# Kernel tuning notes

Measured on AMD Instinct MI355X. Metric: run time of the kernel, lower is better.

The kernel has to match this reference:

```python
import jax, jax.numpy as jnp
import numpy as np

IN_FEATURES = 1024
OUT_FEATURES = 1024
BATCH = 32
SEQ = 1024
EPS = 1e-8


def setup_inputs() -> dict:
    key = jax.random.key(0)
    k1, k2, k3 = jax.random.split(key, 3)
    Efou = jax.random.normal(k1, (BATCH, SEQ, IN_FEATURES), dtype=jnp.float32)
    y = jax.random.normal(k2, (BATCH, IN_FEATURES), dtype=jnp.float32)
    weight = jax.random.normal(k3, (IN_FEATURES, OUT_FEATURES), dtype=jnp.float32)
    return {"Efou": Efou, "y": y, "weight": weight}


def reference(Efou, y, weight):
    # scale = 1/sqrt(in_features)
    scale = 1.0 / np.sqrt(np.float32(weight.shape[0]))
    ys = y * scale  # (b, i) == per-sample column scaling of weight
    # Demodulation norm: sum_i (scale*W[i,o]*y[b,i])^2 = (ys^2) @ (W^2)
    d = jax.lax.rsqrt(jnp.einsum('bi,io->bo', ys * ys, weight * weight) + EPS)  # (b, o)
    # Efou @ (scale*W*y*d) == ((Efou*ys) @ W) * d  -- same math, avoids (b,i,o) weight
    out = jnp.einsum('bsi,io->bso', Efou * ys[:, None, :], weight) * d[:, None, :]
    return out
```

## Files before the change

### kernel.cpp

```cpp
#include <hip/hip_runtime.h>

#define AS1 __attribute__((address_space(1)))
#define AS3 __attribute__((address_space(3)))

typedef __bf16 bf16x8 __attribute__((ext_vector_type(8)));
typedef float f32x4 __attribute__((ext_vector_type(4)));

__device__ __forceinline__ unsigned short f2bf(float f) {
  union { float f; unsigned u; } v; v.f = f;
  unsigned u = v.u;
  unsigned r = (u + 0x7fffu + ((u >> 16) & 1u)) >> 16;
  return (unsigned short)r;
}

__global__ __launch_bounds__(256) void dcalc_a_kernel(const float* __restrict__ y,
                                                      const float* __restrict__ W,
                                                      float* __restrict__ partial) {
  __shared__ float ysq[32][32];
  const int o = blockIdx.x * 256 + threadIdx.x;
  const int i0 = blockIdx.y * 32;
  for (int e = threadIdx.x; e < 1024; e += 256) {
    int il = e >> 5, b = e & 31;
    float t = y[b * 1024 + i0 + il] * 0.03125f;
    ysq[il][b] = t * t;
  }
  __syncthreads();

  f32x4 acc[8] = {};
#pragma unroll
  for (int il = 0; il < 32; ++il) {
    float w = W[(size_t)(i0 + il) * 1024 + o];
    float w2 = w * w;
#pragma unroll
    for (int b4 = 0; b4 < 8; ++b4) {
      f32x4 q = *(const f32x4*)&ysq[il][b4 * 4];
#pragma unroll
      for (int k = 0; k < 4; ++k) acc[b4][k] = fmaf(q[k], w2, acc[b4][k]);
    }
  }
  float* p = partial + (size_t)blockIdx.y * 32768 + o;
#pragma unroll
  for (int b4 = 0; b4 < 8; ++b4)
#pragma unroll
    for (int k = 0; k < 4; ++k) p[(b4 * 4 + k) * 1024] = acc[b4][k];
}

__global__ __launch_bounds__(256) void dcalc_b_kernel(const float* __restrict__ partial,
                                                      float* __restrict__ dmod) {
  const int bo = blockIdx.x * 256 + threadIdx.x;
  float acc = 0.f;
#pragma unroll 8
  for (int is = 0; is < 32; ++is) acc += partial[(size_t)is * 32768 + bo];
  dmod[bo] = rsqrtf(acc + 1e-8f);
}

__global__ void wconv_kernel(const float* __restrict__ W,
                             unsigned short* __restrict__ WT) {
  __shared__ float t[32][33];
  const int tx = threadIdx.x;
  const int ty = threadIdx.y;
  const int i0 = blockIdx.y * 32;
  const int o0 = blockIdx.x * 32;
#pragma unroll
  for (int k = 0; k < 4; ++k)
    t[ty + k * 8][tx] = W[(size_t)(i0 + ty + k * 8) * 1024 + o0 + tx];
  __syncthreads();
#pragma unroll
  for (int k = 0; k < 4; ++k)
    WT[(size_t)(o0 + ty + k * 8) * 1024 + i0 + tx] = f2bf(t[tx][ty + k * 8]);
}

__global__ __launch_bounds__(256) void xconv_kernel(const float4* __restrict__ E4,
                                                    const float* __restrict__ y,
                                                    unsigned short* __restrict__ X) {
  const size_t total = (size_t)8388608;
  for (size_t g = (size_t)blockIdx.x * blockDim.x + threadIdx.x; g < total;
       g += (size_t)gridDim.x * blockDim.x) {
    float4 v = E4[g];
    size_t e = g * 4;
    int i = (int)(e & 1023);
    int b = (int)(e >> 20);
    float4 yv = *(const float4*)(y + b * 1024 + i);
    ushort4 o;
    o.x = f2bf(v.x * yv.x * 0.03125f);
    o.y = f2bf(v.y * yv.y * 0.03125f);
    o.z = f2bf(v.z * yv.z * 0.03125f);
    o.w = f2bf(v.w * yv.w * 0.03125f);
    *(ushort4*)(X + e) = o;
  }
}

#define NT 16
#define LDS_TILE 65536

#define BAR __builtin_amdgcn_s_barrier()
#define LGKM0 asm volatile("s_waitcnt lgkmcnt(0)" ::: "memory")
#define VM(n) asm volatile("s_waitcnt vmcnt(" #n ")" ::: "memory")
#define SCHB __builtin_amdgcn_sched_barrier(0)
#define PRIO(x) __builtin_amdgcn_s_setprio(x)

#define STG_A(r, t, dst)                                                     \
  __builtin_amdgcn_global_load_lds(                                          \
      (const AS1 void*)(Xs + (size_t)(r) * 64 * 2048 + (t) * 128),           \
      (AS3 void*)((dst) + (r) * 8192 + sldso), 16, 0, 0)
#define STG_B(r, t, dst)                                                     \
  __builtin_amdgcn_global_load_lds(                                          \
      (const AS1 void*)(Ws + (size_t)(r) * 64 * 2048 + (t) * 128),           \
      (AS3 void*)((dst) + 32768 + (r) * 8192 + sldso), 16, 0, 0)

#define RD_A(mh, mi, kk)                                                     \
  (*(const bf16x8*)(Ab + (wr * 128 + ((mh) * 4 + (mi)) * 16 + l15) * 128 +   \
                    ((((kk) * 64 + lhi * 16)) ^ swz_rd)))
#define RD_B(nh, ni, kk)                                                     \
  (*(const bf16x8*)(Bb + (wc * 64 + ((nh) * 2 + (ni)) * 16 + l15) * 128 +    \
                    ((((kk) * 64 + lhi * 16)) ^ swz_rd)))

#define LD_A(mh)                                                             \
  { _Pragma("unroll") for (int mi = 0; mi < 4; ++mi)                         \
      _Pragma("unroll") for (int kk = 0; kk < 2; ++kk)                       \
        a[mi][kk] = RD_A(mh, mi, kk); }
#define LD_B(nh)                                                             \
  { _Pragma("unroll") for (int ni = 0; ni < 2; ++ni)                         \
      _Pragma("unroll") for (int kk = 0; kk < 2; ++kk)                       \
        bfr[ni][kk] = RD_B(nh, ni, kk); }

#define MM(mh, nh)                                                           \
  do {                                                                       \
    _Pragma("unroll") for (int mi = 0; mi < 4; ++mi)                         \
      _Pragma("unroll") for (int ni = 0; ni < 2; ++ni)                       \
        _Pragma("unroll") for (int kk = 0; kk < 2; ++kk)                     \
          acc[(mh) * 4 + mi][(nh) * 2 + ni] =                                \
              __builtin_amdgcn_mfma_f32_16x16x32_bf16(                       \
                  a[mi][kk], bfr[ni][kk], acc[(mh) * 4 + mi][(nh) * 2 + ni], \
                  0, 0, 0);                                                  \
  } while (0)

__global__ __launch_bounds__(512, 2) void gemm8_kernel(
    const unsigned short* __restrict__ X, const unsigned short* __restrict__ WT,
    const float* __restrict__ dmod, float* __restrict__ out) {
  extern __shared__ char lds[];
  const int tid = threadIdx.x;
  const int bid = blockIdx.x;
  const int wg = (bid & 7) * 64 + (bid >> 3);
  const int bm = wg >> 2, bn = wg & 3;
  const int m0 = bm * 256, n0 = bn * 256;

  const int w = tid >> 6, l = tid & 63;
  const int wr = w >> 2, wc = w & 3;
  const int l15 = l & 15, lhi = l >> 4;
  const int swz_rd = (l15 & 7) << 4;

  const int srow = tid >> 3;
  const int scb = ((tid & 7) << 4) ^ ((srow & 7) << 4);
  const char* Xs = (const char*)X + (size_t)(m0 + srow) * 2048 + scb;
  const char* Ws = (const char*)WT + (size_t)(n0 + srow) * 2048 + scb;
  const int sldso = tid * 16;

  f32x4 acc[8][4] = {};
  bf16x8 a[4][2], bfr[2][2];

  {
    char* d0 = lds;
    STG_A(0, 0, d0); STG_A(2, 0, d0); STG_B(0, 0, d0); STG_B(1, 0, d0);
    STG_B(2, 0, d0); STG_B(3, 0, d0); STG_A(1, 0, d0); STG_A(3, 0, d0);
  }
  VM(2);
  BAR;

  for (int t = 0; t < NT - 1; ++t) {
    const char* Ab = lds + (t & 1) * LDS_TILE;
    const char* Bb = Ab + 32768;
    char* dN = lds + ((t & 1) ^ 1) * LDS_TILE;
    const int t1 = t + 1;
    LD_A(0); LD_B(0);
    STG_A(0, t1, dN); STG_A(2, t1, dN);
    BAR; LGKM0; SCHB; PRIO(1); MM(0, 0); PRIO(0); SCHB; BAR;
    LD_B(1);
    STG_B(0, t1, dN); STG_B(1, t1, dN);
    BAR; LGKM0; SCHB; PRIO(1); MM(0, 1); PRIO(0); SCHB;
    VM(4);
    BAR;
    LD_A(1); LD_B(0);
    STG_B(2, t1, dN); STG_B(3, t1, dN);
    BAR; LGKM0; SCHB; PRIO(1); MM(1, 0); PRIO(0); SCHB; BAR;
    LD_B(1);
    STG_A(1, t1, dN); STG_A(3, t1, dN);
    BAR; LGKM0; SCHB; PRIO(1); MM(1, 1); PRIO(0); SCHB;
    VM(2);
    BAR;
  }

  {
    const char* Ab = lds + ((NT - 1) & 1) * LDS_TILE;
    const char* Bb = Ab + 32768;
    LD_A(0); LD_B(0);
    BAR; LGKM0; SCHB; PRIO(1); MM(0, 0); PRIO(0); SCHB; BAR;
    LD_B(1);
    BAR; LGKM0; SCHB; PRIO(1); MM(0, 1); PRIO(0); SCHB;
    VM(0);
    BAR;
    LD_A(1); LD_B(0);
    BAR; LGKM0; SCHB; PRIO(1); MM(1, 0); PRIO(0); SCHB; BAR;
    LD_B(1);
    BAR; LGKM0; SCHB; PRIO(1); MM(1, 1); PRIO(0); SCHB;
  }

  const int b = m0 >> 10;
  const int col0 = n0 + wc * 64 + l15;
  float dv[4];
#pragma unroll
  for (int nf = 0; nf < 4; ++nf) dv[nf] = dmod[b * 1024 + col0 + nf * 16];
#pragma unroll
  for (int mf = 0; mf < 8; ++mf) {
#pragma unroll
    for (int j = 0; j < 4; ++j) {
      const int row = m0 + wr * 128 + mf * 16 + lhi * 4 + j;
      float* orow = out + (size_t)row * 1024 + col0;
#pragma unroll
      for (int nf = 0; nf < 4; ++nf) orow[nf * 16] = acc[mf][nf][j] * dv[nf];
    }
  }
}

extern "C" void kernel_launch(void* const* d_in, const int* in_sizes, int n_in,
                              void* d_out, int out_size, void* d_ws, size_t ws_size,
                              hipStream_t stream) {
  const float* Efou = (const float*)d_in[0];
  const float* y    = (const float*)d_in[1];
  const float* W    = (const float*)d_in[2];
  float* out = (float*)d_out;

  unsigned short* X  = (unsigned short*)d_ws;
  unsigned short* WT = X + (size_t)32768 * 1024;
  float* dmod        = (float*)(WT + (size_t)1024 * 1024);
  float* dpart       = dmod + 32768;

  hipFuncSetAttribute((const void*)gemm8_kernel,
                      hipFuncAttributeMaxDynamicSharedMemorySize, 131072);

  dcalc_a_kernel<<<dim3(4, 32), 256, 0, stream>>>(y, W, dpart);
  dcalc_b_kernel<<<128, 256, 0, stream>>>(dpart, dmod);
  wconv_kernel<<<dim3(32, 32), dim3(32, 8), 0, stream>>>(W, WT);
  xconv_kernel<<<2048, 256, 0, stream>>>((const float4*)Efou, y, X);
  gemm8_kernel<<<512, 512, 131072, stream>>>(X, WT, dmod, out);
}
```

Before: 138.9 us.

## Fuse Efou scaling and bf16 conversion into the GEMM A-tile load path

Removes the separate xconv kernel that materialized a scaled bf16 copy of Efou in workspace. The GEMM now loads fp32 Efou rows into registers, multiplies them by the per-batch y scale kept in LDS, converts to bf16 and writes the swizzled A tile to LDS itself. Only the weight tiles still use direct global-to-LDS loads. This drops the write and re-read of the 64 MB intermediate, at the cost of heavier fp32 A traffic per tile (each tile is reread by several column blocks), extra registers, and a full vmcnt(0) wait every iteration that weakens prefetch overlap.

Measured after the change: 129.6 us. -6.7%, faster.

```diff
diff --git a/kernel.cpp b/kernel.cpp
--- a/kernel.cpp
+++ b/kernel.cpp
@@ -5,6 +5,7 @@
 
 typedef __bf16 bf16x8 __attribute__((ext_vector_type(8)));
 typedef float f32x4 __attribute__((ext_vector_type(4)));
+typedef unsigned short ushort8 __attribute__((ext_vector_type(8)));
 
 __device__ __forceinline__ unsigned short f2bf(float f) {
   union { float f; unsigned u; } v; v.f = f;
@@ -70,26 +71,6 @@
     WT[(size_t)(o0 + ty + k * 8) * 1024 + i0 + tx] = f2bf(t[tx][ty + k * 8]);
 }
 
-__global__ __launch_bounds__(256) void xconv_kernel(const float4* __restrict__ E4,
-                                                    const float* __restrict__ y,
-                                                    unsigned short* __restrict__ X) {
-  const size_t total = (size_t)8388608;
-  for (size_t g = (size_t)blockIdx.x * blockDim.x + threadIdx.x; g < total;
-       g += (size_t)gridDim.x * blockDim.x) {
-    float4 v = E4[g];
-    size_t e = g * 4;
-    int i = (int)(e & 1023);
-    int b = (int)(e >> 20);
-    float4 yv = *(const float4*)(y + b * 1024 + i);
-    ushort4 o;
-    o.x = f2bf(v.x * yv.x * 0.03125f);
-    o.y = f2bf(v.y * yv.y * 0.03125f);
-    o.z = f2bf(v.z * yv.z * 0.03125f);
-    o.w = f2bf(v.w * yv.w * 0.03125f);
-    *(ushort4*)(X + e) = o;
-  }
-}
-
 #define NT 16
 #define LDS_TILE 65536
 
@@ -99,14 +80,34 @@
 #define SCHB __builtin_amdgcn_sched_barrier(0)
 #define PRIO(x) __builtin_amdgcn_s_setprio(x)
 
-#define STG_A(r, t, dst)                                                     \
-  __builtin_amdgcn_global_load_lds(                                          \
-      (const AS1 void*)(Xs + (size_t)(r) * 64 * 2048 + (t) * 128),           \
-      (AS3 void*)((dst) + (r) * 8192 + sldso), 16, 0, 0)
 #define STG_B(r, t, dst)                                                     \
   __builtin_amdgcn_global_load_lds(                                          \
       (const AS1 void*)(Ws + (size_t)(r) * 64 * 2048 + (t) * 128),           \
       (AS3 void*)((dst) + 32768 + (r) * 8192 + sldso), 16, 0, 0)
+
+#define A_ISSUE(t)                                                           \
+  {                                                                          \
+    const float* asrc = Efou + (size_t)(m0 + argp * 4) * 1024 + (t) * 64 + k8; \
+    _Pragma("unroll") for (int rr = 0; rr < 4; ++rr) {                       \
+      pa[rr][0] = *(const f32x4*)(asrc + rr * 1024);                         \
+      pa[rr][1] = *(const f32x4*)(asrc + rr * 1024 + 4);                     \
+    }                                                                        \
+    yv[0] = *(const f32x4*)(ysS + (t) * 64 + k8);                            \
+    yv[1] = *(const f32x4*)(ysS + (t) * 64 + k8 + 4);                        \
+  }
+
+#define A_WRITE(dst)                                                         \
+  {                                                                          \
+    _Pragma("unroll") for (int rr = 0; rr < 4; ++rr) {                       \
+      const int row = argp * 4 + rr;                                         \
+      ushort8 ov;                                                            \
+      _Pragma("unroll") for (int q = 0; q < 4; ++q) {                        \
+        ov[q] = f2bf(pa[rr][0][q] * yv[0][q]);                               \
+        ov[q + 4] = f2bf(pa[rr][1][q] * yv[1][q]);                           \
+      }                                                                      \
+      *(ushort8*)((dst) + row * 128 + ((kslot * 16) ^ ((row & 7) << 4))) = ov; \
+    }                                                                        \
+  }
 
 #define RD_A(mh, mi, kk)                                                     \
   (*(const bf16x8*)(Ab + (wr * 128 + ((mh) * 4 + (mi)) * 16 + l15) * 128 +   \
@@ -135,37 +136,51 @@
                   0, 0, 0);                                                  \
   } while (0)
 
-__global__ __launch_bounds__(512, 2) void gemm8_kernel(
-    const unsigned short* __restrict__ X, const unsigned short* __restrict__ WT,
-    const float* __restrict__ dmod, float* __restrict__ out) {
+__global__ __launch_bounds__(512, 2) void gemmf_kernel(
+    const float* __restrict__ Efou, const float* __restrict__ y,
+    const unsigned short* __restrict__ WT, const float* __restrict__ dmod,
+    float* __restrict__ out) {
   extern __shared__ char lds[];
+  float* ysS = (float*)(lds + 2 * LDS_TILE);
+
   const int tid = threadIdx.x;
   const int bid = blockIdx.x;
   const int wg = (bid & 7) * 64 + (bid >> 3);
   const int bm = wg >> 2, bn = wg & 3;
   const int m0 = bm * 256, n0 = bn * 256;
+  const int b = m0 >> 10;
 
   const int w = tid >> 6, l = tid & 63;
   const int wr = w >> 2, wc = w & 3;
   const int l15 = l & 15, lhi = l >> 4;
   const int swz_rd = (l15 & 7) << 4;
 
+  const int kslot = tid & 7;
+  const int k8 = kslot * 8;
+  const int argp = tid >> 3;
+
   const int srow = tid >> 3;
   const int scb = ((tid & 7) << 4) ^ ((srow & 7) << 4);
-  const char* Xs = (const char*)X + (size_t)(m0 + srow) * 2048 + scb;
   const char* Ws = (const char*)WT + (size_t)(n0 + srow) * 2048 + scb;
   const int sldso = tid * 16;
 
   f32x4 acc[8][4] = {};
   bf16x8 a[4][2], bfr[2][2];
-
+  f32x4 pa[4][2], yv[2];
+
+  {
+    float2 yy = *(const float2*)(y + b * 1024 + tid * 2);
+    ysS[2 * tid] = yy.x * 0.03125f;
+    ysS[2 * tid + 1] = yy.y * 0.03125f;
+  }
+  __syncthreads();
   {
     char* d0 = lds;
-    STG_A(0, 0, d0); STG_A(2, 0, d0); STG_B(0, 0, d0); STG_B(1, 0, d0);
-    STG_B(2, 0, d0); STG_B(3, 0, d0); STG_A(1, 0, d0); STG_A(3, 0, d0);
-  }
-  VM(2);
-  BAR;
+    STG_B(0, 0, d0); STG_B(1, 0, d0); STG_B(2, 0, d0); STG_B(3, 0, d0);
+    A_ISSUE(0);
+    A_WRITE(d0);
+  }
+  VM(0); LGKM0; BAR;
 
   for (int t = 0; t < NT - 1; ++t) {
     const char* Ab = lds + (t & 1) * LDS_TILE;
@@ -173,20 +188,19 @@
     char* dN = lds + ((t & 1) ^ 1) * LDS_TILE;
     const int t1 = t + 1;
     LD_A(0); LD_B(0);
-    STG_A(0, t1, dN); STG_A(2, t1, dN);
+    A_ISSUE(t1);
+    STG_B(0, t1, dN); STG_B(1, t1, dN);
     BAR; LGKM0; SCHB; PRIO(1); MM(0, 0); PRIO(0); SCHB; BAR;
     LD_B(1);
-    STG_B(0, t1, dN); STG_B(1, t1, dN);
-    BAR; LGKM0; SCHB; PRIO(1); MM(0, 1); PRIO(0); SCHB;
-    VM(4);
-    BAR;
+    STG_B(2, t1, dN); STG_B(3, t1, dN);
+    BAR; LGKM0; SCHB; PRIO(1); MM(0, 1); PRIO(0); SCHB; BAR;
     LD_A(1); LD_B(0);
-    STG_B(2, t1, dN); STG_B(3, t1, dN);
     BAR; LGKM0; SCHB; PRIO(1); MM(1, 0); PRIO(0); SCHB; BAR;
     LD_B(1);
-    STG_A(1, t1, dN); STG_A(3, t1, dN);
     BAR; LGKM0; SCHB; PRIO(1); MM(1, 1); PRIO(0); SCHB;
-    VM(2);
+    A_WRITE(dN);
+    VM(0);
+    LGKM0;
     BAR;
   }
 
@@ -196,16 +210,13 @@
     LD_A(0); LD_B(0);
     BAR; LGKM0; SCHB; PRIO(1); MM(0, 0); PRIO(0); SCHB; BAR;
     LD_B(1);
-    BAR; LGKM0; SCHB; PRIO(1); MM(0, 1); PRIO(0); SCHB;
-    VM(0);
-    BAR;
+    BAR; LGKM0; SCHB; PRIO(1); MM(0, 1); PRIO(0); SCHB; BAR;
     LD_A(1); LD_B(0);
     BAR; LGKM0; SCHB; PRIO(1); MM(1, 0); PRIO(0); SCHB; BAR;
     LD_B(1);
     BAR; LGKM0; SCHB; PRIO(1); MM(1, 1); PRIO(0); SCHB;
   }
 
-  const int b = m0 >> 10;
   const int col0 = n0 + wc * 64 + l15;
   float dv[4];
 #pragma unroll
@@ -230,17 +241,15 @@
   const float* W    = (const float*)d_in[2];
   float* out = (float*)d_out;
 
-  unsigned short* X  = (unsigned short*)d_ws;
-  unsigned short* WT = X + (size_t)32768 * 1024;
+  unsigned short* WT = (unsigned short*)d_ws;
   float* dmod        = (float*)(WT + (size_t)1024 * 1024);
   float* dpart       = dmod + 32768;
 
-  hipFuncSetAttribute((const void*)gemm8_kernel,
-                      hipFuncAttributeMaxDynamicSharedMemorySize, 131072);
+  hipFuncSetAttribute((const void*)gemmf_kernel,
+                      hipFuncAttributeMaxDynamicSharedMemorySize, 135168);
 
   dcalc_a_kernel<<<dim3(4, 32), 256, 0, stream>>>(y, W, dpart);
   dcalc_b_kernel<<<128, 256, 0, stream>>>(dpart, dmod);
   wconv_kernel<<<dim3(32, 32), dim3(32, 8), 0, stream>>>(W, WT);
-  xconv_kernel<<<2048, 256, 0, stream>>>((const float4*)Efou, y, X);
-  gemm8_kernel<<<512, 512, 131072, stream>>>(X, WT, dmod, out);
-}
+  gemmf_kernel<<<512, 512, 135168, stream>>>(Efou, y, WT, dmod, out);
+}
```

## Prefetch A tiles two steps ahead and B one step in GEMM pipeline

Applied to the files above, without the earlier changes.

Restructures the GEMM's double-buffered LDS schedule so the A operand tile is staged two K-steps ahead, into the half of the current buffer already consumed, while B is staged one step ahead. The prologue now preloads tile 0 plus the A part of tile 1, and the loop is split into a main body, an NT-2 peeled step and a final step. The goal is more time for global loads to land before they are needed, hiding memory latency. The risk is that writing A into the buffer still being read relies on the barrier placement to avoid overwriting data in use, and the extra loads in flight raise vmcnt pressure.

Result: no change. 138.6 us (-0.2%).

```diff
diff --git a/kernel.cpp b/kernel.cpp
--- a/kernel.cpp
+++ b/kernel.cpp
@@ -135,7 +135,7 @@
                   0, 0, 0);                                                  \
   } while (0)
 
-__global__ __launch_bounds__(512, 2) void gemm8_kernel(
+__global__ __launch_bounds__(512, 2) void gemm8d_kernel(
     const unsigned short* __restrict__ X, const unsigned short* __restrict__ WT,
     const float* __restrict__ dmod, float* __restrict__ out) {
   extern __shared__ char lds[];
@@ -159,34 +159,55 @@
   f32x4 acc[8][4] = {};
   bf16x8 a[4][2], bfr[2][2];
 
-  {
-    char* d0 = lds;
-    STG_A(0, 0, d0); STG_A(2, 0, d0); STG_B(0, 0, d0); STG_B(1, 0, d0);
-    STG_B(2, 0, d0); STG_B(3, 0, d0); STG_A(1, 0, d0); STG_A(3, 0, d0);
-  }
-  VM(2);
+  char* buf0 = lds;
+  char* buf1 = lds + LDS_TILE;
+
+  STG_A(0, 0, buf0); STG_A(2, 0, buf0); STG_A(1, 0, buf0); STG_A(3, 0, buf0);
+  STG_B(0, 0, buf0); STG_B(1, 0, buf0); STG_B(2, 0, buf0); STG_B(3, 0, buf0);
+  STG_A(0, 1, buf1); STG_A(2, 1, buf1); STG_A(1, 1, buf1); STG_A(3, 1, buf1);
+  VM(4);
   BAR;
 
-  for (int t = 0; t < NT - 1; ++t) {
+  for (int t = 0; t < NT - 2; ++t) {
     const char* Ab = lds + (t & 1) * LDS_TILE;
     const char* Bb = Ab + 32768;
-    char* dN = lds + ((t & 1) ^ 1) * LDS_TILE;
+    char* dB = lds + ((t + 1) & 1) * LDS_TILE;
+    char* dA = lds + (t & 1) * LDS_TILE;
+    const int t1 = t + 1, t2 = t + 2;
+    const bool stA = (t2 < NT);
+    LD_A(0); LD_B(0);
+    STG_B(0, t1, dB); STG_B(1, t1, dB);
+    BAR; LGKM0; SCHB; PRIO(1); MM(0, 0); PRIO(0); SCHB; BAR;
+    LD_B(1);
+    STG_B(2, t1, dB); STG_B(3, t1, dB);
+    BAR; LGKM0; SCHB; PRIO(1); MM(0, 1); PRIO(0); SCHB; BAR;
+    LD_A(1); LD_B(0);
+    if (stA) { STG_A(0, t2, dA); STG_A(2, t2, dA); }
+    BAR; LGKM0; SCHB; PRIO(1); MM(1, 0); PRIO(0); SCHB; BAR;
+    LD_B(1);
+    if (stA) { STG_A(1, t2, dA); STG_A(3, t2, dA); }
+    BAR; LGKM0; SCHB; PRIO(1); MM(1, 1); PRIO(0); SCHB;
+    VM(4);
+    BAR;
+  }
+
+  {
+    const int t = NT - 2;
+    const char* Ab = lds + (t & 1) * LDS_TILE;
+    const char* Bb = Ab + 32768;
+    char* dB = lds + ((t + 1) & 1) * LDS_TILE;
     const int t1 = t + 1;
     LD_A(0); LD_B(0);
-    STG_A(0, t1, dN); STG_A(2, t1, dN);
+    STG_B(0, t1, dB); STG_B(1, t1, dB);
     BAR; LGKM0; SCHB; PRIO(1); MM(0, 0); PRIO(0); SCHB; BAR;
     LD_B(1);
-    STG_B(0, t1, dN); STG_B(1, t1, dN);
-    BAR; LGKM0; SCHB; PRIO(1); MM(0, 1); PRIO(0); SCHB;
-    VM(4);
-    BAR;
+    STG_B(2, t1, dB); STG_B(3, t1, dB);
+    BAR; LGKM0; SCHB; PRIO(1); MM(0, 1); PRIO(0); SCHB; BAR;
     LD_A(1); LD_B(0);
-    STG_B(2, t1, dN); STG_B(3, t1, dN);
     BAR; LGKM0; SCHB; PRIO(1); MM(1, 0); PRIO(0); SCHB; BAR;
     LD_B(1);
-    STG_A(1, t1, dN); STG_A(3, t1, dN);
     BAR; LGKM0; SCHB; PRIO(1); MM(1, 1); PRIO(0); SCHB;
-    VM(2);
+    VM(0);
     BAR;
   }
 
@@ -196,9 +217,7 @@
     LD_A(0); LD_B(0);
     BAR; LGKM0; SCHB; PRIO(1); MM(0, 0); PRIO(0); SCHB; BAR;
     LD_B(1);
-    BAR; LGKM0; SCHB; PRIO(1); MM(0, 1); PRIO(0); SCHB;
-    VM(0);
-    BAR;
+    BAR; LGKM0; SCHB; PRIO(1); MM(0, 1); PRIO(0); SCHB; BAR;
     LD_A(1); LD_B(0);
     BAR; LGKM0; SCHB; PRIO(1); MM(1, 0); PRIO(0); SCHB; BAR;
     LD_B(1);
@@ -235,12 +254,12 @@
   float* dmod        = (float*)(WT + (size_t)1024 * 1024);
   float* dpart       = dmod + 32768;
 
-  hipFuncSetAttribute((const void*)gemm8_kernel,
+  hipFuncSetAttribute((const void*)gemm8d_kernel,
                       hipFuncAttributeMaxDynamicSharedMemorySize, 131072);
 
   dcalc_a_kernel<<<dim3(4, 32), 256, 0, stream>>>(y, W, dpart);
   dcalc_b_kernel<<<128, 256, 0, stream>>>(dpart, dmod);
   wconv_kernel<<<dim3(32, 32), dim3(32, 8), 0, stream>>>(W, WT);
   xconv_kernel<<<2048, 256, 0, stream>>>((const float4*)Efou, y, X);
-  gemm8_kernel<<<512, 512, 131072, stream>>>(X, WT, dmod, out);
-}
+  gemm8d_kernel<<<512, 512, 131072, stream>>>(X, WT, dmod, out);
+}
```

## Process two N-tiles per workgroup in one continuous K pipeline

Applied to the files above, without the earlier changes.

Each workgroup now computes a 256x512 output strip as two consecutive 256x256 tiles, streaming 32 K-steps through one pipeline so the prologue and drain happen once per pair. The MFMA operands are swapped so each lane holds four consecutive columns, which allows vectorized f32x4 output stores. The demodulation factors are staged in LDS. Occupancy drops to one 512-thread workgroup per CU, and the grid halves to 256 blocks, which may leave some CUs idle or hide latency less well.

Measured after the change: 144.1 us. 1.04x slower.

```diff
diff --git a/kernel.cpp b/kernel.cpp
--- a/kernel.cpp
+++ b/kernel.cpp
@@ -90,7 +90,6 @@
   }
 }
 
-#define NT 16
 #define LDS_TILE 65536
 
 #define BAR __builtin_amdgcn_s_barrier()
@@ -99,13 +98,13 @@
 #define SCHB __builtin_amdgcn_sched_barrier(0)
 #define PRIO(x) __builtin_amdgcn_s_setprio(x)
 
-#define STG_A(r, t, dst)                                                     \
+#define STG_A(r, kt, dst)                                                    \
   __builtin_amdgcn_global_load_lds(                                          \
-      (const AS1 void*)(Xs + (size_t)(r) * 64 * 2048 + (t) * 128),           \
+      (const AS1 void*)(Xs + (size_t)(r) * 64 * 2048 + (kt) * 128),          \
       (AS3 void*)((dst) + (r) * 8192 + sldso), 16, 0, 0)
-#define STG_B(r, t, dst)                                                     \
+#define STG_B(r, kt, dst, WsB)                                               \
   __builtin_amdgcn_global_load_lds(                                          \
-      (const AS1 void*)(Ws + (size_t)(r) * 64 * 2048 + (t) * 128),           \
+      (const AS1 void*)((WsB) + (size_t)(r) * 64 * 2048 + (kt) * 128),       \
       (AS3 void*)((dst) + 32768 + (r) * 8192 + sldso), 16, 0, 0)
 
 #define RD_A(mh, mi, kk)                                                     \
@@ -122,7 +121,7 @@
 #define LD_B(nh)                                                             \
   { _Pragma("unroll") for (int ni = 0; ni < 2; ++ni)                         \
       _Pragma("unroll") for (int kk = 0; kk < 2; ++kk)                       \
-        bfr[ni][kk] = RD_B(nh, ni, kk); }
+        bfr[nh][ni][kk] = RD_B(nh, ni, kk); }
 
 #define MM(mh, nh)                                                           \
   do {                                                                       \
@@ -131,19 +130,62 @@
         _Pragma("unroll") for (int kk = 0; kk < 2; ++kk)                     \
           acc[(mh) * 4 + mi][(nh) * 2 + ni] =                                \
               __builtin_amdgcn_mfma_f32_16x16x32_bf16(                       \
-                  a[mi][kk], bfr[ni][kk], acc[(mh) * 4 + mi][(nh) * 2 + ni], \
-                  0, 0, 0);                                                  \
+                  bfr[nh][ni][kk], a[mi][kk],                                \
+                  acc[(mh) * 4 + mi][(nh) * 2 + ni], 0, 0, 0);               \
   } while (0)
 
-__global__ __launch_bounds__(512, 2) void gemm8_kernel(
+#define STEADY(tt)                                                           \
+  {                                                                          \
+    const char* Ab = lds + ((tt) & 1) * LDS_TILE;                            \
+    const char* Bb = Ab + 32768;                                             \
+    char* dB = lds + (((tt) + 1) & 1) * LDS_TILE;                            \
+    char* dA = lds + ((tt) & 1) * LDS_TILE;                                  \
+    const char* WsB = ((((tt) + 1) >> 4) ? Ws1 : Ws0);                       \
+    const int ktB = ((tt) + 1) & 15, ktA = ((tt) + 2) & 15;                  \
+    LD_A(0); LD_B(0);                                                        \
+    STG_B(0, ktB, dB, WsB); STG_B(1, ktB, dB, WsB);                          \
+    BAR; LGKM0; SCHB; PRIO(1); MM(0, 0); PRIO(0); SCHB; BAR;                 \
+    LD_B(1);                                                                 \
+    STG_B(2, ktB, dB, WsB); STG_B(3, ktB, dB, WsB);                          \
+    BAR; LGKM0; SCHB; PRIO(1); MM(0, 1); PRIO(0); SCHB; BAR;                 \
+    LD_A(1);                                                                 \
+    STG_A(0, ktA, dA); STG_A(2, ktA, dA);                                    \
+    BAR; LGKM0; SCHB; PRIO(1); MM(1, 0); PRIO(0); SCHB; BAR;                 \
+    STG_A(1, ktA, dA); STG_A(3, ktA, dA);                                    \
+    BAR; LGKM0; SCHB; PRIO(1); MM(1, 1); PRIO(0); SCHB;                      \
+    VM(4); BAR;                                                              \
+  }
+
+#define EPI(p)                                                               \
+  {                                                                          \
+    const int ob = wc * 64 + lhi * 4;                                        \
+    _Pragma("unroll") for (int on = 0; on < 4; ++on) {                       \
+      f32x4 dv = *(const f32x4*)(dtab + (p) * 256 + ob + on * 16);           \
+      _Pragma("unroll") for (int am = 0; am < 8; ++am) {                     \
+        const int m = m0 + wr * 128 + am * 16 + l15;                         \
+        f32x4 v;                                                             \
+        _Pragma("unroll") for (int j = 0; j < 4; ++j)                        \
+          v[j] = acc[am][on][j] * dv[j];                                     \
+        *(f32x4*)(out + (size_t)m * 1024 + n0base + (p) * 256 + ob +         \
+                  on * 16) = v;                                              \
+      }                                                                      \
+    }                                                                        \
+  }
+
+__global__ __launch_bounds__(512, 1) void gemmp_kernel(
     const unsigned short* __restrict__ X, const unsigned short* __restrict__ WT,
     const float* __restrict__ dmod, float* __restrict__ out) {
   extern __shared__ char lds[];
+  float* dtab = (float*)(lds + 2 * LDS_TILE);
+
   const int tid = threadIdx.x;
   const int bid = blockIdx.x;
-  const int wg = (bid & 7) * 64 + (bid >> 3);
-  const int bm = wg >> 2, bn = wg & 3;
-  const int m0 = bm * 256, n0 = bn * 256;
+  const int wg = (bid & 7) * 32 + (bid >> 3);
+  const int bm = wg >> 1;
+  const int pairp = wg & 1;
+  const int m0 = bm * 256;
+  const int n0base = pairp * 512;
+  const int b = m0 >> 10;
 
   const int w = tid >> 6, l = tid & 63;
   const int wr = w >> 2, wc = w & 3;
@@ -153,73 +195,65 @@
   const int srow = tid >> 3;
   const int scb = ((tid & 7) << 4) ^ ((srow & 7) << 4);
   const char* Xs = (const char*)X + (size_t)(m0 + srow) * 2048 + scb;
-  const char* Ws = (const char*)WT + (size_t)(n0 + srow) * 2048 + scb;
+  const char* Ws0 = (const char*)WT + (size_t)(n0base + srow) * 2048 + scb;
+  const char* Ws1 = Ws0 + (size_t)256 * 2048;
   const int sldso = tid * 16;
 
   f32x4 acc[8][4] = {};
-  bf16x8 a[4][2], bfr[2][2];
+  bf16x8 a[4][2], bfr[2][2][2];
+
+  char* buf0 = lds;
+  char* buf1 = lds + LDS_TILE;
+
+  dtab[tid] = dmod[b * 1024 + n0base + tid];
+  __syncthreads();
+
+  STG_A(0, 0, buf0); STG_A(2, 0, buf0); STG_A(1, 0, buf0); STG_A(3, 0, buf0);
+  STG_B(0, 0, buf0, Ws0); STG_B(1, 0, buf0, Ws0);
+  STG_B(2, 0, buf0, Ws0); STG_B(3, 0, buf0, Ws0);
+  STG_A(0, 1, buf1); STG_A(2, 1, buf1); STG_A(1, 1, buf1); STG_A(3, 1, buf1);
+  VM(4);
+  BAR;
+
+  for (int tt = 0; tt < 16; ++tt) STEADY(tt);
+
+  EPI(0);
+#pragma unroll
+  for (int am = 0; am < 8; ++am)
+#pragma unroll
+    for (int on = 0; on < 4; ++on) acc[am][on] = (f32x4){0.f, 0.f, 0.f, 0.f};
+
+  for (int tt = 16; tt < 30; ++tt) STEADY(tt);
 
   {
-    char* d0 = lds;
-    STG_A(0, 0, d0); STG_A(2, 0, d0); STG_B(0, 0, d0); STG_B(1, 0, d0);
-    STG_B(2, 0, d0); STG_B(3, 0, d0); STG_A(1, 0, d0); STG_A(3, 0, d0);
-  }
-  VM(2);
-  BAR;
-
-  for (int t = 0; t < NT - 1; ++t) {
-    const char* Ab = lds + (t & 1) * LDS_TILE;
+    const char* Ab = lds + (30 & 1) * LDS_TILE;
     const char* Bb = Ab + 32768;
-    char* dN = lds + ((t & 1) ^ 1) * LDS_TILE;
-    const int t1 = t + 1;
+    char* dB = lds + (31 & 1) * LDS_TILE;
     LD_A(0); LD_B(0);
-    STG_A(0, t1, dN); STG_A(2, t1, dN);
+    STG_B(0, 15, dB, Ws1); STG_B(1, 15, dB, Ws1);
     BAR; LGKM0; SCHB; PRIO(1); MM(0, 0); PRIO(0); SCHB; BAR;
     LD_B(1);
-    STG_B(0, t1, dN); STG_B(1, t1, dN);
-    BAR; LGKM0; SCHB; PRIO(1); MM(0, 1); PRIO(0); SCHB;
-    VM(4);
-    BAR;
-    LD_A(1); LD_B(0);
-    STG_B(2, t1, dN); STG_B(3, t1, dN);
+    STG_B(2, 15, dB, Ws1); STG_B(3, 15, dB, Ws1);
+    BAR; LGKM0; SCHB; PRIO(1); MM(0, 1); PRIO(0); SCHB; BAR;
+    LD_A(1);
     BAR; LGKM0; SCHB; PRIO(1); MM(1, 0); PRIO(0); SCHB; BAR;
-    LD_B(1);
-    STG_A(1, t1, dN); STG_A(3, t1, dN);
     BAR; LGKM0; SCHB; PRIO(1); MM(1, 1); PRIO(0); SCHB;
-    VM(2);
-    BAR;
+    VM(0); BAR;
   }
 
   {
-    const char* Ab = lds + ((NT - 1) & 1) * LDS_TILE;
+    const char* Ab = lds + (31 & 1) * LDS_TILE;
     const char* Bb = Ab + 32768;
     LD_A(0); LD_B(0);
     BAR; LGKM0; SCHB; PRIO(1); MM(0, 0); PRIO(0); SCHB; BAR;
     LD_B(1);
-    BAR; LGKM0; SCHB; PRIO(1); MM(0, 1); PRIO(0); SCHB;
-    VM(0);
-    BAR;
-    LD_A(1); LD_B(0);
+    BAR; LGKM0; SCHB; PRIO(1); MM(0, 1); PRIO(0); SCHB; BAR;
+    LD_A(1);
     BAR; LGKM0; SCHB; PRIO(1); MM(1, 0); PRIO(0); SCHB; BAR;
-    LD_B(1);
     BAR; LGKM0; SCHB; PRIO(1); MM(1, 1); PRIO(0); SCHB;
   }
 
-  const int b = m0 >> 10;
-  const int col0 = n0 + wc * 64 + l15;
-  float dv[4];
-#pragma unroll
-  for (int nf = 0; nf < 4; ++nf) dv[nf] = dmod[b * 1024 + col0 + nf * 16];
-#pragma unroll
-  for (int mf = 0; mf < 8; ++mf) {
-#pragma unroll
-    for (int j = 0; j < 4; ++j) {
-      const int row = m0 + wr * 128 + mf * 16 + lhi * 4 + j;
-      float* orow = out + (size_t)row * 1024 + col0;
-#pragma unroll
-      for (int nf = 0; nf < 4; ++nf) orow[nf * 16] = acc[mf][nf][j] * dv[nf];
-    }
-  }
+  EPI(1);
 }
 
 extern "C" void kernel_launch(void* const* d_in, const int* in_sizes, int n_in,
@@ -235,12 +269,12 @@
   float* dmod        = (float*)(WT + (size_t)1024 * 1024);
   float* dpart       = dmod + 32768;
 
-  hipFuncSetAttribute((const void*)gemm8_kernel,
-                      hipFuncAttributeMaxDynamicSharedMemorySize, 131072);
+  hipFuncSetAttribute((const void*)gemmp_kernel,
+                      hipFuncAttributeMaxDynamicSharedMemorySize, 133120);
 
   dcalc_a_kernel<<<dim3(4, 32), 256, 0, stream>>>(y, W, dpart);
   dcalc_b_kernel<<<128, 256, 0, stream>>>(dpart, dmod);
   wconv_kernel<<<dim3(32, 32), dim3(32, 8), 0, stream>>>(W, WT);
   xconv_kernel<<<2048, 256, 0, stream>>>((const float4*)Efou, y, X);
-  gemm8_kernel<<<512, 512, 131072, stream>>>(X, WT, dmod, out);
-}
+  gemmp_kernel<<<256, 512, 133120, stream>>>(X, WT, dmod, out);
+}
```
